# Kernel optimization log

Hardware: AMD Instinct MI355X
Metric: run time of the kernel (lower is better)

## Reference

```python
import jax, jax.numpy as jnp
import numpy as np

NEG_SLOPE = 0.01  # torch LeakyReLU default
BN_EPS = 1e-5     # torch BatchNorm1d default


def _bn(x, g, b):
    # training-mode batch norm over the node axis
    m = jnp.mean(x, axis=0)
    v = jnp.var(x, axis=0)
    return g * (x - m) * jax.lax.rsqrt(v + BN_EPS) + b


def _lrelu(x):
    return jax.nn.leaky_relu(x, NEG_SLOPE)


def setup_inputs() -> dict:
    key = jax.random.key(0)
    N, E, W, D = 100_000, 1_600_000, 32, 10
    ks = iter(jax.random.split(key, 64))

    def w(shape):
        fan_in = shape[-2] if len(shape) >= 2 else shape[-1]
        return (jax.random.normal(next(ks), shape, jnp.float32) / np.sqrt(fan_in)).astype(jnp.float32)

    inp = {}
    inp["x"] = jax.random.normal(next(ks), (N, 1), jnp.float32)
    inp["col_e_idx"] = jax.random.randint(next(ks), (2, E), 0, N, dtype=jnp.int32)
    # init_node_feature_trans: MLP 1 -> [32] -> 32, LeakyReLU, batch_norm=True
    inp["Wi0"] = w((1, W)); inp["bi0"] = jnp.zeros(W); inp["gi0"] = jnp.ones(W); inp["bei0"] = jnp.zeros(W)
    inp["Wi1"] = w((W, W)); inp["bi1"] = jnp.zeros(W); inp["gi1"] = jnp.ones(W); inp["bei1"] = jnp.zeros(W)
    # 10 CollConv layers (identical dims -> stacked params)
    inp["Wm"] = w((D, W, W)); inp["bm"] = jnp.zeros((D, W)); inp["gm"] = jnp.ones((D, W)); inp["bem"] = jnp.zeros((D, W))
    inp["Wu"] = w((D, 2 * W, W)); inp["bu"] = jnp.zeros((D, W)); inp["gu"] = jnp.ones((D, W)); inp["beu"] = jnp.zeros((D, W))
    # final_mlp: 32 -> 256 -> 128 -> 64 -> 32 (LeakyReLU, no BN), then 32 -> 1 sigmoid
    inp["Wf0"] = w((W, 256)); inp["bf0"] = jnp.zeros(256)
    inp["Wf1"] = w((256, 128)); inp["bf1"] = jnp.zeros(128)
    inp["Wf2"] = w((128, 64)); inp["bf2"] = jnp.zeros(64)
    inp["Wf3"] = w((64, W)); inp["bf3"] = jnp.zeros(W)
    inp["Wo"] = w((W, 1)); inp["bo"] = jnp.zeros(1)
    return inp


def reference(x, col_e_idx, Wi0, bi0, gi0, bei0, Wi1, bi1, gi1, bei1,
              Wm, bm, gm, bem, Wu, bu, gu, beu,
              Wf0, bf0, Wf1, bf1, Wf2, bf2, Wf3, bf3, Wo, bo):
    N = x.shape[0]
    D = Wm.shape[0]
    src, dst = col_e_idx[0], col_e_idx[1]

    # init node-feature MLP (Linear -> BN -> LeakyReLU, twice)
    h = _lrelu(_bn(x @ Wi0 + bi0, gi0, bei0))
    h = _lrelu(_bn(h @ Wi1 + bi1, gi1, bei1))

    feats = [h]  # middle_features[0]
    for i in range(D):  # fixed small depth -> python loop is fine
        # CollConv: node-wise message transform, edge gather, scatter-sum, update
        msg = _lrelu(_bn(h @ Wm[i] + bm[i], gm[i], bem[i]))      # [N, W]
        agg = jax.ops.segment_sum(msg[src], dst, num_segments=N)  # [N, W]
        h = _lrelu(_bn(jnp.concatenate([h, agg], axis=-1) @ Wu[i] + bu[i], gu[i], beu[i]))
        if i - 2 >= 0:  # residual_skip_num = 2
            h = h + feats[i - 2]
        feats.append(h)

    # final MLP (no BN) + sigmoid head
    h = _lrelu(h @ Wf0 + bf0)
    h = _lrelu(h @ Wf1 + bf1)
    h = _lrelu(h @ Wf2 + bf2)
    h = _lrelu(h @ Wf3 + bf3)
    return jax.nn.sigmoid(h @ Wo + bo)  # [N, 1]
```

## Files before the change

### kernel.cpp

```cpp
#include <hip/hip_runtime.h>
#include <hip/hip_bf16.h>

#define NN 100000
#define NEDGE 1600000
#define NV (NN*32)
#define NEG 0.01f
#define EPS 1e-5f
#define NBLK 391
#define NBKT 391
#define CHUNK 4096
#define NCBLK 391
#define DCAP 6144
#define STC 64
#define ST_STRIDE 4096

#define OFF_STATS 0
#define STATS_F  (22*ST_STRIDE)
#define OFF_PA   STATS_F
#define OFF_PB   (OFF_PA + NV)
#define OFF_AGG  (OFF_PB + NV)
#define OFF_MSGB (OFF_AGG + NV)
#define OFF_RING (OFF_MSGB + NV/2)
#define OFF_WF   (OFF_RING + 4*NV)
#define ARENA_F  (OFF_WF + 25600)

#define W0B 0
#define W1B 1024
#define W2B 5120
#define W3B 6144

__device__ __align__(16) float gA[ARENA_F];
__device__ int g_rowptr[NN + 1];
__device__ int g_csr[NEDGE];
__device__ int g_bin[NEDGE];
__device__ int g_bcnt[NBKT];
__device__ int g_boff[NBKT];
__device__ int g_btail[NBKT];

__device__ __forceinline__ float lrelu(float v) { return v > 0.f ? v : v * NEG; }
__device__ __forceinline__ unsigned short f2b(float v) {
    __hip_bfloat16 b = __float2bfloat16(v);
    return *reinterpret_cast<unsigned short*>(&b);
}
__device__ __forceinline__ float b2f(unsigned short u) {
    __hip_bfloat16 b = *reinterpret_cast<__hip_bfloat16*>(&u);
    return __bfloat162float(b);
}

__global__ void k_zero_v19()
{
    int i = blockIdx.x * 256 + threadIdx.x;
    if (i < STATS_F) gA[i] = 0.f;
    if (i < NBKT) g_bcnt[i] = 0;
}

__global__ __launch_bounds__(256) void k_bcnt_v19(const int* __restrict__ col)
{
    __shared__ int hist[NBKT];
    int tid = threadIdx.x;
    for (int b = tid; b < NBKT; b += 256) hist[b] = 0;
    __syncthreads();
    int e0 = blockIdx.x * CHUNK;
    #pragma unroll
    for (int r = 0; r < CHUNK / 256; ++r) {
        int e = e0 + r * 256 + tid;
        if (e < NEDGE) atomicAdd(&hist[col[NEDGE + e] >> 8], 1);
    }
    __syncthreads();
    for (int b = tid; b < NBKT; b += 256) {
        int v = hist[b];
        if (v) atomicAdd(&g_bcnt[b], v);
    }
}

__global__ __launch_bounds__(512) void k_bscan_v19()
{
    __shared__ int s[512];
    int t = threadIdx.x;
    int v = (t < NBKT) ? g_bcnt[t] : 0;
    s[t] = v;
    __syncthreads();
    for (int off = 1; off < 512; off <<= 1) {
        int u = (t >= off) ? s[t - off] : 0;
        __syncthreads();
        s[t] += u;
        __syncthreads();
    }
    if (t < NBKT) {
        int o = s[t] - v;
        g_boff[t] = o;
        g_btail[t] = o;
    }
}

__global__ __launch_bounds__(256) void k_binfill_v19(const int* __restrict__ col)
{
    __shared__ int ssrc[CHUNK];
    __shared__ int sdst[CHUNK];
    __shared__ int hist[NBKT];
    __shared__ int boffL[NBKT];
    __shared__ int cnt2[NBKT];
    int tid = threadIdx.x;
    for (int b = tid; b < NBKT; b += 256) { hist[b] = 0; cnt2[b] = 0; }
    __syncthreads();
    int e0 = blockIdx.x * CHUNK;
    #pragma unroll
    for (int r = 0; r < CHUNK / 256; ++r) {
        int i = r * 256 + tid;
        int e = e0 + i;
        if (e < NEDGE) {
            int s = col[e];
            int d = col[NEDGE + e];
            ssrc[i] = s;
            sdst[i] = d;
            atomicAdd(&hist[d >> 8], 1);
        }
    }
    __syncthreads();
    for (int b = tid; b < NBKT; b += 256) {
        int h = hist[b];
        if (h) boffL[b] = atomicAdd(&g_btail[b], h);
    }
    __syncthreads();
    #pragma unroll
    for (int r = 0; r < CHUNK / 256; ++r) {
        int i = r * 256 + tid;
        int e = e0 + i;
        if (e < NEDGE) {
            int d = sdst[i];
            int b = d >> 8;
            int rk = atomicAdd(&cnt2[b], 1);
            g_bin[boffL[b] + rk] = (ssrc[i] << 8) | (d & 255);
        }
    }
}

__global__ __launch_bounds__(256) void k_csr_v19()
{
    __shared__ int stg[DCAP];
    __shared__ int c1[256];
    __shared__ int sc[256];
    __shared__ int sl[256];
    __shared__ int c2[256];
    int tid = threadIdx.x, b = blockIdx.x;
    int base = g_boff[b];
    int cntE = g_bcnt[b];
    c1[tid] = 0; c2[tid] = 0;
    __syncthreads();
    for (int i = tid; i < cntE; i += 256) {
        int p = g_bin[base + i];
        if (i < DCAP) stg[i] = p;
        atomicAdd(&c1[p & 255], 1);
    }
    __syncthreads();
    int v = c1[tid];
    sc[tid] = v;
    __syncthreads();
    for (int off = 1; off < 256; off <<= 1) {
        int u = (tid >= off) ? sc[tid - off] : 0;
        __syncthreads();
        sc[tid] += u;
        __syncthreads();
    }
    int loff = sc[tid] - v;
    sl[tid] = loff;
    int node = b * 256 + tid;
    if (node < NN) g_rowptr[node] = base + loff;
    if (b == NBKT - 1 && tid == 0) g_rowptr[NN] = NEDGE;
    __syncthreads();
    for (int i = tid; i < cntE; i += 256) {
        int p = (i < DCAP) ? stg[i] : g_bin[base + i];
        int dl = p & 255;
        int rk = atomicAdd(&c2[dl], 1);
        g_csr[base + sl[dl] + rk] = p >> 8;
    }
}

__global__ void k_init0_v17(const float* __restrict__ x, const float* __restrict__ Wi0,
                            const float* __restrict__ bi0)
{
    int j = threadIdx.x & 31, ns = threadIdx.x >> 5;
    float w = Wi0[j];
    float bb = bi0[j];
    __shared__ float red[64];
    if (threadIdx.x < 64) red[threadIdx.x] = 0.f;
    __syncthreads();
    float s1 = 0.f, s2 = 0.f;
    for (int t = blockIdx.x; t < NN / 8; t += gridDim.x) {
        int n = t * 8 + ns;
        float v = x[n] * w + bb;
        gA[OFF_PA + n * 32 + j] = v;
        s1 += v; s2 += v * v;
    }
    atomicAdd(&red[j], s1);
    atomicAdd(&red[j + 32], s2);
    __syncthreads();
    if (threadIdx.x < 64)
        atomicAdd(&gA[OFF_STATS + (blockIdx.x & (STC - 1)) * 64 + threadIdx.x], red[threadIdx.x]);
}

__global__ void k_nl_v17(int off_in, int off_out, int out_msg, int st_in,
                         const float* __restrict__ gamma, const float* __restrict__ beta,
                         int off_resid, int off_feats,
                         const float* __restrict__ Wn, const float* __restrict__ bn,
                         int st_out)
{
    int j = threadIdx.x & 31, ns = threadIdx.x >> 5;
    __shared__ float sstat[64];
    __shared__ float red[64];
    if (threadIdx.x < 64) {
        red[threadIdx.x] = 0.f;
        float acc = 0.f;
        int base = st_in + threadIdx.x;
        #pragma unroll 8
        for (int c = 0; c < STC; ++c) acc += gA[base + c * 64];
        sstat[threadIdx.x] = acc;
    }
    __syncthreads();
    float mean = sstat[j] * (1.f / NN);
    float var  = sstat[32 + j] * (1.f / NN) - mean * mean;
    float scale = gamma[j] * rsqrtf(var + EPS);
    float shift = beta[j] - mean * scale;

    float wc[32]; float bb = 0.f;
    if (Wn) {
        #pragma unroll
        for (int k = 0; k < 32; ++k) wc[k] = Wn[k * 32 + j];
        bb = bn[j];
    }
    unsigned short* mb = (unsigned short*)(gA + OFF_MSGB);
    __shared__ float sH[8][32];
    float s1 = 0.f, s2 = 0.f;
    for (int t = blockIdx.x; t < NN / 8; t += gridDim.x) {
        int n = t * 8 + ns;
        float v = gA[off_in + n * 32 + j];
        v = lrelu(scale * v + shift);
        if (off_resid >= 0) v += gA[off_resid + n * 32 + j];
        if (off_feats >= 0) gA[off_feats + n * 32 + j] = v;
        if (Wn) {
            sH[ns][j] = v;
            __syncthreads();
            float acc = bb;
            #pragma unroll
            for (int k = 0; k < 32; k += 4) {
                float4 h4 = *(const float4*)&sH[ns][k];
                acc += h4.x * wc[k] + h4.y * wc[k + 1] + h4.z * wc[k + 2] + h4.w * wc[k + 3];
            }
            if (out_msg) mb[n * 32 + j] = f2b(acc);
            else gA[off_out + n * 32 + j] = acc;
            s1 += acc; s2 += acc * acc;
            __syncthreads();
        }
    }
    if (Wn) {
        atomicAdd(&red[j], s1);
        atomicAdd(&red[j + 32], s2);
        __syncthreads();
        if (threadIdx.x < 64)
            atomicAdd(&gA[st_out + (blockIdx.x & (STC - 1)) * 64 + threadIdx.x], red[threadIdx.x]);
    }
}

__global__ __launch_bounds__(256) void k_gather_v17(int st,
                                                    const float* __restrict__ gm,
                                                    const float* __restrict__ bem)
{
    __shared__ float sstat[64];
    __shared__ float sc[32], sh[32];
    int tid = threadIdx.x;
    if (tid < 64) {
        float acc = 0.f;
        int base = st + tid;
        #pragma unroll 8
        for (int c = 0; c < STC; ++c) acc += gA[base + c * 64];
        sstat[tid] = acc;
    }
    __syncthreads();
    if (tid < 32) {
        float mean = sstat[tid] * (1.f / NN);
        float var  = sstat[32 + tid] * (1.f / NN) - mean * mean;
        float s = gm[tid] * rsqrtf(var + EPS);
        sc[tid] = s;
        sh[tid] = bem[tid] - mean * s;
    }
    __syncthreads();
    int n = blockIdx.x * 32 + (tid >> 3);
    int g = tid & 7;
    int e0 = g_rowptr[n], e1 = g_rowptr[n + 1];
    const unsigned short* mb = (const unsigned short*)(gA + OFF_MSGB);
    float c0 = sc[g*4], c1 = sc[g*4+1], c2 = sc[g*4+2], c3 = sc[g*4+3];
    float h0 = sh[g*4], h1 = sh[g*4+1], h2 = sh[g*4+2], h3 = sh[g*4+3];
    float a0 = 0.f, a1 = 0.f, a2 = 0.f, a3 = 0.f;
    int e = e0;
    for (; e + 3 < e1; e += 4) {
        int s0 = g_csr[e];
        int s1 = g_csr[e + 1];
        int s2 = g_csr[e + 2];
        int s3 = g_csr[e + 3];
        ushort4 m0 = *(const ushort4*)(mb + s0 * 32 + g * 4);
        ushort4 m1 = *(const ushort4*)(mb + s1 * 32 + g * 4);
        ushort4 m2 = *(const ushort4*)(mb + s2 * 32 + g * 4);
        ushort4 m3 = *(const ushort4*)(mb + s3 * 32 + g * 4);
        a0 += lrelu(c0 * b2f(m0.x) + h0) + lrelu(c0 * b2f(m1.x) + h0)
            + lrelu(c0 * b2f(m2.x) + h0) + lrelu(c0 * b2f(m3.x) + h0);
        a1 += lrelu(c1 * b2f(m0.y) + h1) + lrelu(c1 * b2f(m1.y) + h1)
            + lrelu(c1 * b2f(m2.y) + h1) + lrelu(c1 * b2f(m3.y) + h1);
        a2 += lrelu(c2 * b2f(m0.z) + h2) + lrelu(c2 * b2f(m1.z) + h2)
            + lrelu(c2 * b2f(m2.z) + h2) + lrelu(c2 * b2f(m3.z) + h2);
        a3 += lrelu(c3 * b2f(m0.w) + h3) + lrelu(c3 * b2f(m1.w) + h3)
            + lrelu(c3 * b2f(m2.w) + h3) + lrelu(c3 * b2f(m3.w) + h3);
    }
    for (; e < e1; ++e) {
        int s0 = g_csr[e];
        ushort4 m0 = *(const ushort4*)(mb + s0 * 32 + g * 4);
        a0 += lrelu(c0 * b2f(m0.x) + h0);
        a1 += lrelu(c1 * b2f(m0.y) + h1);
        a2 += lrelu(c2 * b2f(m0.z) + h2);
        a3 += lrelu(c3 * b2f(m0.w) + h3);
    }
    *(float4*)(gA + OFF_AGG + n * 32 + g * 4) = make_float4(a0, a1, a2, a3);
}

__global__ void k_upd_v17(int off_h, int off_out,
                          const float* __restrict__ Wu_i, const float* __restrict__ bu_i,
                          int st_out)
{
    int j = threadIdx.x & 31, ns = threadIdx.x >> 5;
    float wc[64];
    #pragma unroll
    for (int k = 0; k < 64; ++k) wc[k] = Wu_i[k * 32 + j];
    float bb = bu_i[j];
    __shared__ float sH[8][32];
    __shared__ float sA[8][32];
    __shared__ float red[64];
    if (threadIdx.x < 64) red[threadIdx.x] = 0.f;
    __syncthreads();
    float s1 = 0.f, s2 = 0.f;
    for (int t = blockIdx.x; t < NN / 8; t += gridDim.x) {
        int n = t * 8 + ns;
        sH[ns][j] = gA[off_h + n * 32 + j];
        sA[ns][j] = gA[OFF_AGG + n * 32 + j];
        __syncthreads();
        float acc = bb;
        #pragma unroll
        for (int k = 0; k < 32; k += 4) {
            float4 h4 = *(const float4*)&sH[ns][k];
            acc += h4.x * wc[k] + h4.y * wc[k + 1] + h4.z * wc[k + 2] + h4.w * wc[k + 3];
            float4 a4 = *(const float4*)&sA[ns][k];
            acc += a4.x * wc[32 + k] + a4.y * wc[32 + k + 1] + a4.z * wc[32 + k + 2] + a4.w * wc[32 + k + 3];
        }
        gA[off_out + n * 32 + j] = acc;
        s1 += acc; s2 += acc * acc;
        __syncthreads();
    }
    atomicAdd(&red[j], s1);
    atomicAdd(&red[j + 32], s2);
    __syncthreads();
    if (threadIdx.x < 64)
        atomicAdd(&gA[st_out + (blockIdx.x & (STC - 1)) * 64 + threadIdx.x], red[threadIdx.x]);
}


typedef __attribute__((ext_vector_type(8))) short bf16x8;
typedef __attribute__((ext_vector_type(4))) float f32x4;

union FC { uint4 u; bf16x8 b; };

#define MFMA(a, b, c) __builtin_amdgcn_mfma_f32_16x16x32_bf16(a, b, c, 0, 0, 0)

__device__ __forceinline__ bf16x8 ld_wf(const uint4* p) {
    FC c; c.u = *p; return c.b;
}

__device__ __forceinline__ f32x4 ld_bias4(const float* p) {
    float4 t = *(const float4*)p;
    f32x4 r; r[0] = t.x; r[1] = t.y; r[2] = t.z; r[3] = t.w; return r;
}

__device__ __forceinline__ f32x4 lrelu4(f32x4 v) {
    f32x4 r;
    #pragma unroll
    for (int k = 0; k < 4; ++k) r[k] = v[k] > 0.f ? v[k] : v[k] * NEG;
    return r;
}

__device__ __forceinline__ void splitpack(const float* v, bf16x8& hi, bf16x8& lo) {
    unsigned int h[4], l[4];
    #pragma unroll
    for (int k = 0; k < 4; ++k) {
        unsigned short h0 = f2b(v[2*k]), h1 = f2b(v[2*k+1]);
        float r0 = v[2*k]   - b2f(h0);
        float r1 = v[2*k+1] - b2f(h1);
        h[k] = (unsigned int)h0 | ((unsigned int)h1 << 16);
        l[k] = (unsigned int)f2b(r0) | ((unsigned int)f2b(r1) << 16);
    }
    FC ch; ch.u = make_uint4(h[0], h[1], h[2], h[3]); hi = ch.b;
    FC cl; cl.u = make_uint4(l[0], l[1], l[2], l[3]); lo = cl.b;
}

__global__ __launch_bounds__(256) void k_wprep_v18(const float* __restrict__ W0,
                                                   const float* __restrict__ W1,
                                                   const float* __restrict__ W2,
                                                   const float* __restrict__ W3)
{
    int i = blockIdx.x * 256 + threadIdx.x;
    if (i >= 51200) return;
    const float* src; int Nout, nk; int r = i;
    if (r < 8192)       { src = W0; Nout = 256; nk = 1; }
    else if (r < 40960) { src = W1; Nout = 128; nk = 8; r -= 8192; }
    else if (r < 49152) { src = W2; Nout = 64;  nk = 4; r -= 40960; }
    else                { src = W3; Nout = 32;  nk = 2; r -= 49152; }
    int frag = r >> 9;
    int lane = (r >> 3) & 63;
    int j = r & 7;
    int T = frag / nk, s = frag - T * nk;
    int g = lane >> 4;
    int outf = T * 16 + (lane & 15);
    int inf = 32 * s + 16 * (j >> 2) + 4 * g + (j & 3);
    unsigned short* dst = (unsigned short*)(gA + OFF_WF);
    dst[i] = f2b(src[inf * Nout + outf]);
}

__global__ __launch_bounds__(256) void k_final_v18(
    int off_h,
    const float* __restrict__ bf0, const float* __restrict__ bf1,
    const float* __restrict__ bf2, const float* __restrict__ bf3,
    const float* __restrict__ Wo,  const float* __restrict__ bo,
    float* __restrict__ out)
{
    int lane = threadIdx.x & 63;
    int wave = threadIdx.x >> 6;
    int c = lane & 15;
    int g = lane >> 4;
    int nb = blockIdx.x * 128 + wave * 32;
    int n0 = nb + c;
    int n1 = nb + 16 + c;
    int ld0 = min(n0, NN - 1), ld1 = min(n1, NN - 1);

    const float* h = gA + off_h;
    const uint4* WF = (const uint4*)(gA + OFF_WF);

    float4 ia0 = *(const float4*)&h[ld0 * 32 + 4 * g];
    float4 ib0 = *(const float4*)&h[ld0 * 32 + 16 + 4 * g];
    float4 ia1 = *(const float4*)&h[ld1 * 32 + 4 * g];
    float4 ib1 = *(const float4*)&h[ld1 * 32 + 16 + 4 * g];
    bf16x8 Bh0, Bl0, Bh1, Bl1;
    {
        float v0[8] = {ia0.x, ia0.y, ia0.z, ia0.w, ib0.x, ib0.y, ib0.z, ib0.w};
        float v1[8] = {ia1.x, ia1.y, ia1.z, ia1.w, ib1.x, ib1.y, ib1.z, ib1.w};
        splitpack(v0, Bh0, Bl0);
        splitpack(v1, Bh1, Bl1);
    }

    f32x4 A0[16][2];
    #pragma unroll
    for (int t = 0; t < 16; ++t) {
        f32x4 ci = ld_bias4(bf0 + t * 16 + 4 * g);
        bf16x8 w = ld_wf(WF + W0B + t * 64 + lane);
        f32x4 d0 = MFMA(w, Bh0, ci);
        d0 = MFMA(w, Bl0, d0);
        f32x4 d1 = MFMA(w, Bh1, ci);
        d1 = MFMA(w, Bl1, d1);
        A0[t][0] = lrelu4(d0);
        A0[t][1] = lrelu4(d1);
    }

    f32x4 A1[8][2];
    #pragma unroll
    for (int T = 0; T < 8; ++T) {
        f32x4 ci = ld_bias4(bf1 + T * 16 + 4 * g);
        A1[T][0] = ci; A1[T][1] = ci;
    }
    #pragma unroll
    for (int s = 0; s < 8; ++s) {
        bf16x8 bh[2], bl[2];
        #pragma unroll
        for (int u = 0; u < 2; ++u) {
            float vv[8] = {A0[2*s][u][0], A0[2*s][u][1], A0[2*s][u][2], A0[2*s][u][3],
                           A0[2*s+1][u][0], A0[2*s+1][u][1], A0[2*s+1][u][2], A0[2*s+1][u][3]};
            splitpack(vv, bh[u], bl[u]);
        }
        #pragma unroll
        for (int T = 0; T < 8; ++T) {
            bf16x8 w = ld_wf(WF + W1B + (T * 8 + s) * 64 + lane);
            A1[T][0] = MFMA(w, bh[0], A1[T][0]);
            A1[T][0] = MFMA(w, bl[0], A1[T][0]);
            A1[T][1] = MFMA(w, bh[1], A1[T][1]);
            A1[T][1] = MFMA(w, bl[1], A1[T][1]);
        }
    }
    #pragma unroll
    for (int T = 0; T < 8; ++T) { A1[T][0] = lrelu4(A1[T][0]); A1[T][1] = lrelu4(A1[T][1]); }

    f32x4 A2[4][2];
    #pragma unroll
    for (int T = 0; T < 4; ++T) {
        f32x4 ci = ld_bias4(bf2 + T * 16 + 4 * g);
        A2[T][0] = ci; A2[T][1] = ci;
    }
    #pragma unroll
    for (int s = 0; s < 4; ++s) {
        bf16x8 bh[2], bl[2];
        #pragma unroll
        for (int u = 0; u < 2; ++u) {
            float vv[8] = {A1[2*s][u][0], A1[2*s][u][1], A1[2*s][u][2], A1[2*s][u][3],
                           A1[2*s+1][u][0], A1[2*s+1][u][1], A1[2*s+1][u][2], A1[2*s+1][u][3]};
            splitpack(vv, bh[u], bl[u]);
        }
        #pragma unroll
        for (int T = 0; T < 4; ++T) {
            bf16x8 w = ld_wf(WF + W2B + (T * 4 + s) * 64 + lane);
            A2[T][0] = MFMA(w, bh[0], A2[T][0]);
            A2[T][0] = MFMA(w, bl[0], A2[T][0]);
            A2[T][1] = MFMA(w, bh[1], A2[T][1]);
            A2[T][1] = MFMA(w, bl[1], A2[T][1]);
        }
    }
    #pragma unroll
    for (int T = 0; T < 4; ++T) { A2[T][0] = lrelu4(A2[T][0]); A2[T][1] = lrelu4(A2[T][1]); }

    f32x4 A3[2][2];
    #pragma unroll
    for (int T = 0; T < 2; ++T) {
        f32x4 ci = ld_bias4(bf3 + T * 16 + 4 * g);
        A3[T][0] = ci; A3[T][1] = ci;
    }
    #pragma unroll
    for (int s = 0; s < 2; ++s) {
        bf16x8 bh[2], bl[2];
        #pragma unroll
        for (int u = 0; u < 2; ++u) {
            float vv[8] = {A2[2*s][u][0], A2[2*s][u][1], A2[2*s][u][2], A2[2*s][u][3],
                           A2[2*s+1][u][0], A2[2*s+1][u][1], A2[2*s+1][u][2], A2[2*s+1][u][3]};
            splitpack(vv, bh[u], bl[u]);
        }
        #pragma unroll
        for (int T = 0; T < 2; ++T) {
            bf16x8 w = ld_wf(WF + W3B + (T * 2 + s) * 64 + lane);
            A3[T][0] = MFMA(w, bh[0], A3[T][0]);
            A3[T][0] = MFMA(w, bl[0], A3[T][0]);
            A3[T][1] = MFMA(w, bh[1], A3[T][1]);
            A3[T][1] = MFMA(w, bl[1], A3[T][1]);
        }
    }
    #pragma unroll
    for (int T = 0; T < 2; ++T) { A3[T][0] = lrelu4(A3[T][0]); A3[T][1] = lrelu4(A3[T][1]); }

    float4 woa = *(const float4*)&Wo[4 * g];
    float4 wob = *(const float4*)&Wo[16 + 4 * g];
    float z0 = A3[0][0][0]*woa.x + A3[0][0][1]*woa.y + A3[0][0][2]*woa.z + A3[0][0][3]*woa.w
             + A3[1][0][0]*wob.x + A3[1][0][1]*wob.y + A3[1][0][2]*wob.z + A3[1][0][3]*wob.w;
    float z1 = A3[0][1][0]*woa.x + A3[0][1][1]*woa.y + A3[0][1][2]*woa.z + A3[0][1][3]*woa.w
             + A3[1][1][0]*wob.x + A3[1][1][1]*wob.y + A3[1][1][2]*wob.z + A3[1][1][3]*wob.w;
    z0 += __shfl_xor(z0, 16); z0 += __shfl_xor(z0, 32);
    z1 += __shfl_xor(z1, 16); z1 += __shfl_xor(z1, 32);
    float bb = bo[0];
    if (g == 0 && n0 < NN) out[n0] = 1.f / (1.f + __expf(-(z0 + bb)));
    if (g == 1 && n1 < NN) out[n1] = 1.f / (1.f + __expf(-(z1 + bb)));
}

extern "C" void kernel_launch(void* const* d_in, const int* in_sizes, int n_in,
                              void* d_out, int out_size, void* d_ws, size_t ws_size,
                              hipStream_t stream)
{
    (void)in_sizes; (void)n_in; (void)out_size; (void)d_ws; (void)ws_size;
    float* out = (float*)d_out;

    const float* x   = (const float*)d_in[0];
    const int*  col  = (const int*) d_in[1];
    const float* Wi0 = (const float*)d_in[2];
    const float* bi0 = (const float*)d_in[3];
    const float* gi0 = (const float*)d_in[4];
    const float* bei0= (const float*)d_in[5];
    const float* Wi1 = (const float*)d_in[6];
    const float* bi1 = (const float*)d_in[7];
    const float* gi1 = (const float*)d_in[8];
    const float* bei1= (const float*)d_in[9];
    const float* Wm  = (const float*)d_in[10];
    const float* bm  = (const float*)d_in[11];
    const float* gm  = (const float*)d_in[12];
    const float* bem = (const float*)d_in[13];
    const float* Wu  = (const float*)d_in[14];
    const float* bu  = (const float*)d_in[15];
    const float* gu  = (const float*)d_in[16];
    const float* beu = (const float*)d_in[17];
    const float* Wf0 = (const float*)d_in[18];
    const float* bf0 = (const float*)d_in[19];
    const float* Wf1 = (const float*)d_in[20];
    const float* bf1 = (const float*)d_in[21];
    const float* Wf2 = (const float*)d_in[22];
    const float* bf2 = (const float*)d_in[23];
    const float* Wf3 = (const float*)d_in[24];
    const float* bf3 = (const float*)d_in[25];
    const float* Wo  = (const float*)d_in[26];
    const float* bo  = (const float*)d_in[27];

    const int st_i0 = OFF_STATS;
    const int st_i1 = OFF_STATS + ST_STRIDE;
    const int st_m  = OFF_STATS + 2 * ST_STRIDE;
    const int st_u  = OFF_STATS + 12 * ST_STRIDE;

    const int RING[4] = { OFF_RING, OFF_RING + NV, OFF_RING + 2 * NV, OFF_RING + 3 * NV };

    dim3 blk(256);
    k_zero_v19<<<NBLK, blk, 0, stream>>>();
    k_bcnt_v19<<<NCBLK, blk, 0, stream>>>(col);
    k_bscan_v19<<<1, 512, 0, stream>>>();
    k_binfill_v19<<<NCBLK, blk, 0, stream>>>(col);
    k_csr_v19<<<NBKT, blk, 0, stream>>>();
    k_wprep_v18<<<200, blk, 0, stream>>>(Wf0, Wf1, Wf2, Wf3);

    k_init0_v17<<<1024, blk, 0, stream>>>(x, Wi0, bi0);
    k_nl_v17<<<1024, blk, 0, stream>>>(OFF_PA, OFF_PB, 0, st_i0, gi0, bei0, -1, -1, Wi1, bi1, st_i1);
    k_nl_v17<<<1024, blk, 0, stream>>>(OFF_PB, 0, 1, st_i1, gi1, bei1, -1, RING[0], Wm, bm, st_m);

    for (int i = 0; i < 10; ++i) {
        int h_cur = RING[i & 3];
        int h_new = RING[(i + 1) & 3];
        int resid = (i >= 2) ? RING[(i - 2) & 3] : -1;
        k_gather_v17<<<3125, blk, 0, stream>>>(st_m + i * ST_STRIDE, gm + i * 32, bem + i * 32);
        k_upd_v17<<<1024, blk, 0, stream>>>(h_cur, OFF_PB, Wu + i * 2048, bu + i * 32,
                                            st_u + i * ST_STRIDE);
        const float* Wn = (i < 9) ? (Wm + (i + 1) * 1024) : nullptr;
        const float* bn = (i < 9) ? (bm + (i + 1) * 32) : nullptr;
        int st_next = (i < 9) ? (st_m + (i + 1) * ST_STRIDE) : 0;
        k_nl_v17<<<1024, blk, 0, stream>>>(OFF_PB, 0, 1, st_u + i * ST_STRIDE,
                                           gu + i * 32, beu + i * 32,
                                           resid, h_new, Wn, bn, st_next);
    }

    k_final_v18<<<782, blk, 0, stream>>>(RING[2], bf0, bf1, bf2, bf3, Wo, bo, out);
}
```

Measured before the change: 978.3 us.

## Fuse edge gather and update linear into one kernel per layer

```diff
diff --git a/kernel.cpp b/kernel.cpp
--- a/kernel.cpp
+++ b/kernel.cpp
@@ -13,6 +13,7 @@
 #define DCAP 6144
 #define STC 64
 #define ST_STRIDE 4096
+#define NGBLK 1563
 
 #define OFF_STATS 0
 #define STATS_F  (22*ST_STRIDE)
@@ -261,105 +262,130 @@
     }
 }
 
-__global__ __launch_bounds__(256) void k_gather_v17(int st,
-                                                    const float* __restrict__ gm,
-                                                    const float* __restrict__ bem)
+__global__ __launch_bounds__(256) void k_gupd_v20(int st_msg,
+                                                  const float* __restrict__ gm,
+                                                  const float* __restrict__ bem,
+                                                  int off_h,
+                                                  const float* __restrict__ Wu_i,
+                                                  const float* __restrict__ bu_i,
+                                                  int st_out)
 {
     __shared__ float sstat[64];
-    __shared__ float sc[32], sh[32];
+    __shared__ float scl[32], shf[32];
+    __shared__ float sH[64][36];
+    __shared__ float sAgg[64][36];
+    __shared__ float red[64];
     int tid = threadIdx.x;
+    int nb = blockIdx.x * 64;
+
     if (tid < 64) {
+        red[tid] = 0.f;
         float acc = 0.f;
-        int base = st + tid;
+        int base = st_msg + tid;
         #pragma unroll 8
         for (int c = 0; c < STC; ++c) acc += gA[base + c * 64];
         sstat[tid] = acc;
+    }
+    {
+        const float* hp = gA + off_h + nb * 32;
+        int lim = min(2048, (NN - nb) * 32);
+        for (int idx = tid; idx < lim; idx += 256)
+            sH[idx >> 5][idx & 31] = hp[idx];
     }
     __syncthreads();
     if (tid < 32) {
         float mean = sstat[tid] * (1.f / NN);
         float var  = sstat[32 + tid] * (1.f / NN) - mean * mean;
         float s = gm[tid] * rsqrtf(var + EPS);
-        sc[tid] = s;
-        sh[tid] = bem[tid] - mean * s;
-    }
-    __syncthreads();
-    int n = blockIdx.x * 32 + (tid >> 3);
-    int g = tid & 7;
-    int e0 = g_rowptr[n], e1 = g_rowptr[n + 1];
-    const unsigned short* mb = (const unsigned short*)(gA + OFF_MSGB);
-    float c0 = sc[g*4], c1 = sc[g*4+1], c2 = sc[g*4+2], c3 = sc[g*4+3];
-    float h0 = sh[g*4], h1 = sh[g*4+1], h2 = sh[g*4+2], h3 = sh[g*4+3];
-    float a0 = 0.f, a1 = 0.f, a2 = 0.f, a3 = 0.f;
-    int e = e0;
-    for (; e + 3 < e1; e += 4) {
-        int s0 = g_csr[e];
-        int s1 = g_csr[e + 1];
-        int s2 = g_csr[e + 2];
-        int s3 = g_csr[e + 3];
-        ushort4 m0 = *(const ushort4*)(mb + s0 * 32 + g * 4);
-        ushort4 m1 = *(const ushort4*)(mb + s1 * 32 + g * 4);
-        ushort4 m2 = *(const ushort4*)(mb + s2 * 32 + g * 4);
-        ushort4 m3 = *(const ushort4*)(mb + s3 * 32 + g * 4);
-        a0 += lrelu(c0 * b2f(m0.x) + h0) + lrelu(c0 * b2f(m1.x) + h0)
-            + lrelu(c0 * b2f(m2.x) + h0) + lrelu(c0 * b2f(m3.x) + h0);
-        a1 += lrelu(c1 * b2f(m0.y) + h1) + lrelu(c1 * b2f(m1.y) + h1)
-            + lrelu(c1 * b2f(m2.y) + h1) + lrelu(c1 * b2f(m3.y) + h1);
-        a2 += lrelu(c2 * b2f(m0.z) + h2) + lrelu(c2 * b2f(m1.z) + h2)
-            + lrelu(c2 * b2f(m2.z) + h2) + lrelu(c2 * b2f(m3.z) + h2);
-        a3 += lrelu(c3 * b2f(m0.w) + h3) + lrelu(c3 * b2f(m1.w) + h3)
-            + lrelu(c3 * b2f(m2.w) + h3) + lrelu(c3 * b2f(m3.w) + h3);
-    }
-    for (; e < e1; ++e) {
-        int s0 = g_csr[e];
-        ushort4 m0 = *(const ushort4*)(mb + s0 * 32 + g * 4);
-        a0 += lrelu(c0 * b2f(m0.x) + h0);
-        a1 += lrelu(c1 * b2f(m0.y) + h1);
-        a2 += lrelu(c2 * b2f(m0.z) + h2);
-        a3 += lrelu(c3 * b2f(m0.w) + h3);
-    }
-    *(float4*)(gA + OFF_AGG + n * 32 + g * 4) = make_float4(a0, a1, a2, a3);
-}
-
-__global__ void k_upd_v17(int off_h, int off_out,
-                          const float* __restrict__ Wu_i, const float* __restrict__ bu_i,
-                          int st_out)
-{
-    int j = threadIdx.x & 31, ns = threadIdx.x >> 5;
-    float wc[64];
-    #pragma unroll
-    for (int k = 0; k < 64; ++k) wc[k] = Wu_i[k * 32 + j];
-    float bb = bu_i[j];
-    __shared__ float sH[8][32];
-    __shared__ float sA[8][32];
-    __shared__ float red[64];
-    if (threadIdx.x < 64) red[threadIdx.x] = 0.f;
-    __syncthreads();
-    float s1 = 0.f, s2 = 0.f;
-    for (int t = blockIdx.x; t < NN / 8; t += gridDim.x) {
-        int n = t * 8 + ns;
-        sH[ns][j] = gA[off_h + n * 32 + j];
-        sA[ns][j] = gA[OFF_AGG + n * 32 + j];
+        scl[tid] = s;
+        shf[tid] = bem[tid] - mean * s;
+    }
+    __syncthreads();
+
+    {
+        int nl = tid >> 2;
+        int g  = tid & 3;
+        int n  = nb + nl;
+        float c[8], h[8];
+        #pragma unroll
+        for (int q = 0; q < 8; ++q) { c[q] = scl[g * 8 + q]; h[q] = shf[g * 8 + q]; }
+        float a[8];
+        #pragma unroll
+        for (int q = 0; q < 8; ++q) a[q] = 0.f;
+        if (n < NN) {
+            const unsigned short* mb = (const unsigned short*)(gA + OFF_MSGB);
+            int e0 = g_rowptr[n], e1 = g_rowptr[n + 1];
+            int e = e0;
+            for (; e + 3 < e1; e += 4) {
+                int s0 = g_csr[e];
+                int s1 = g_csr[e + 1];
+                int s2 = g_csr[e + 2];
+                int s3 = g_csr[e + 3];
+                uint4 m0 = *(const uint4*)(mb + (s0 << 5) + (g << 3));
+                uint4 m1 = *(const uint4*)(mb + (s1 << 5) + (g << 3));
+                uint4 m2 = *(const uint4*)(mb + (s2 << 5) + (g << 3));
+                uint4 m3 = *(const uint4*)(mb + (s3 << 5) + (g << 3));
+                #pragma unroll
+                for (int w = 0; w < 4; ++w) {
+                    unsigned int u0 = (&m0.x)[w], u1 = (&m1.x)[w], u2 = (&m2.x)[w], u3 = (&m3.x)[w];
+                    int q = w * 2;
+                    a[q]   += lrelu(c[q]   * b2f((unsigned short)(u0 & 0xffff)) + h[q])
+                            + lrelu(c[q]   * b2f((unsigned short)(u1 & 0xffff)) + h[q])
+                            + lrelu(c[q]   * b2f((unsigned short)(u2 & 0xffff)) + h[q])
+                            + lrelu(c[q]   * b2f((unsigned short)(u3 & 0xffff)) + h[q]);
+                    a[q+1] += lrelu(c[q+1] * b2f((unsigned short)(u0 >> 16)) + h[q+1])
+                            + lrelu(c[q+1] * b2f((unsigned short)(u1 >> 16)) + h[q+1])
+                            + lrelu(c[q+1] * b2f((unsigned short)(u2 >> 16)) + h[q+1])
+                            + lrelu(c[q+1] * b2f((unsigned short)(u3 >> 16)) + h[q+1]);
+                }
+            }
+            for (; e < e1; ++e) {
+                int s0 = g_csr[e];
+                uint4 m0 = *(const uint4*)(mb + (s0 << 5) + (g << 3));
+                #pragma unroll
+                for (int w = 0; w < 4; ++w) {
+                    unsigned int u0 = (&m0.x)[w];
+                    int q = w * 2;
+                    a[q]   += lrelu(c[q]   * b2f((unsigned short)(u0 & 0xffff)) + h[q]);
+                    a[q+1] += lrelu(c[q+1] * b2f((unsigned short)(u0 >> 16)) + h[q+1]);
+                }
+            }
+        }
+        *(float4*)&sAgg[nl][g * 8]     = make_float4(a[0], a[1], a[2], a[3]);
+        *(float4*)&sAgg[nl][g * 8 + 4] = make_float4(a[4], a[5], a[6], a[7]);
+    }
+    __syncthreads();
+
+    {
+        int j = tid & 31, ns = tid >> 5;
+        float wc[64];
+        #pragma unroll
+        for (int k = 0; k < 64; ++k) wc[k] = Wu_i[k * 32 + j];
+        float bb = bu_i[j];
+        float s1 = 0.f, s2 = 0.f;
+        #pragma unroll
+        for (int it = 0; it < 8; ++it) {
+            int nl = it * 8 + ns;
+            int n = nb + nl;
+            if (n >= NN) break;
+            float acc = bb;
+            #pragma unroll
+            for (int k = 0; k < 32; k += 4) {
+                float4 h4 = *(const float4*)&sH[nl][k];
+                acc += h4.x * wc[k] + h4.y * wc[k + 1] + h4.z * wc[k + 2] + h4.w * wc[k + 3];
+                float4 a4 = *(const float4*)&sAgg[nl][k];
+                acc += a4.x * wc[32 + k] + a4.y * wc[32 + k + 1] + a4.z * wc[32 + k + 2] + a4.w * wc[32 + k + 3];
+            }
+            gA[OFF_PB + n * 32 + j] = acc;
+            s1 += acc; s2 += acc * acc;
+        }
+        atomicAdd(&red[j], s1);
+        atomicAdd(&red[j + 32], s2);
         __syncthreads();
-        float acc = bb;
-        #pragma unroll
-        for (int k = 0; k < 32; k += 4) {
-            float4 h4 = *(const float4*)&sH[ns][k];
-            acc += h4.x * wc[k] + h4.y * wc[k + 1] + h4.z * wc[k + 2] + h4.w * wc[k + 3];
-            float4 a4 = *(const float4*)&sA[ns][k];
-            acc += a4.x * wc[32 + k] + a4.y * wc[32 + k + 1] + a4.z * wc[32 + k + 2] + a4.w * wc[32 + k + 3];
-        }
-        gA[off_out + n * 32 + j] = acc;
-        s1 += acc; s2 += acc * acc;
-        __syncthreads();
-    }
-    atomicAdd(&red[j], s1);
-    atomicAdd(&red[j + 32], s2);
-    __syncthreads();
-    if (threadIdx.x < 64)
-        atomicAdd(&gA[st_out + (blockIdx.x & (STC - 1)) * 64 + threadIdx.x], red[threadIdx.x]);
-}
-
+        if (tid < 64)
+            atomicAdd(&gA[st_out + (blockIdx.x & (STC - 1)) * 64 + tid], red[tid]);
+    }
+}
 
 typedef __attribute__((ext_vector_type(8))) short bf16x8;
 typedef __attribute__((ext_vector_type(4))) float f32x4;
@@ -618,9 +644,9 @@
         int h_cur = RING[i & 3];
         int h_new = RING[(i + 1) & 3];
         int resid = (i >= 2) ? RING[(i - 2) & 3] : -1;
-        k_gather_v17<<<3125, blk, 0, stream>>>(st_m + i * ST_STRIDE, gm + i * 32, bem + i * 32);
-        k_upd_v17<<<1024, blk, 0, stream>>>(h_cur, OFF_PB, Wu + i * 2048, bu + i * 32,
-                                            st_u + i * ST_STRIDE);
+        k_gupd_v20<<<NGBLK, blk, 0, stream>>>(st_m + i * ST_STRIDE, gm + i * 32, bem + i * 32,
+                                              h_cur, Wu + i * 2048, bu + i * 32,
+                                              st_u + i * ST_STRIDE);
         const float* Wn = (i < 9) ? (Wm + (i + 1) * 1024) : nullptr;
         const float* bn = (i < 9) ? (bm + (i + 1) * 32) : nullptr;
         int st_next = (i < 9) ? (st_m + (i + 1) * ST_STRIDE) : 0;
```

Result: no change. 966.8 us (-1.2%).
